# Performance work log

Hardware: AMD Instinct MI355X
Metric: run time of the kernel (lower is better)

The kernel has to match this reference:

```python
import jax, jax.numpy as jnp
import numpy as np

L1, L2, B, D1, D2, HEADS, M = 1024, 1024, 8, 512, 1024, 16, 1024
DPH = M // HEADS  # 64


def setup_inputs() -> dict:
    key = jax.random.key(0)
    ks = jax.random.split(key, 10)
    w = lambda k, shp: jax.random.normal(k, shp, jnp.float32) * 0.02
    z = lambda n: jnp.zeros((n,), jnp.float32)
    return {
        "ctx_1": jax.random.normal(ks[0], (L1, B, D1), jnp.float32),
        "ctx_2": jax.random.normal(ks[1], (L2, B, D2), jnp.float32),
        "Wk1": w(ks[2], (M, D1)), "bk1": z(M),
        "Wv1": w(ks[3], (M, D1)), "bv1": z(M),
        "Wk2": w(ks[4], (M, D2)), "bk2": z(M),
        "Wv2": w(ks[5], (M, D2)), "bv2": z(M),
        "Wf12": w(ks[6], (M, M)), "bf12": z(M),
        "Wf21": w(ks[7], (M, M)), "bf21": z(M),
    }


def _shape_heads(x):
    # [L, B, M] -> [B, H, L, dph]
    L, Bs, _ = x.shape
    return x.reshape(L, Bs, HEADS, DPH).transpose(1, 2, 0, 3)


def _unshape(x):
    # [B, H, L, dph] -> [L, B, M]
    Bs, Hn, L, d = x.shape
    return x.transpose(2, 0, 1, 3).reshape(L, Bs, Hn * d)


def reference(ctx_1, ctx_2, Wk1, bk1, Wv1, bv1, Wk2, bk2, Wv2, bv2,
              Wf12, bf12, Wf21, bf21):
    k1 = _shape_heads(ctx_1 @ Wk1.T + bk1)  # [B,H,L1,d]
    v1 = _shape_heads(ctx_1 @ Wv1.T + bv1)  # [B,H,L1,d]
    k2 = _shape_heads(ctx_2 @ Wk2.T + bk2)  # [B,H,L2,d]
    v2 = _shape_heads(ctx_2 @ Wv2.T + bv2)  # [B,H,L2,d]

    # scores: key_2 @ key_1^T -> [B, H, L2, L1]
    scores = jnp.einsum('bhqd,bhkd->bhqk', k2, k1)

    # direction 1 -> 2: softmax over dim=2 (the L2 axis), then AV with value_1
    dist_1_to_2 = jax.nn.softmax(scores, axis=2)
    context_1_to_2 = jnp.einsum('bhqk,bhkd->bhqd', dist_1_to_2, v1)  # [B,H,L2,d]
    context_1_to_2 = _unshape(context_1_to_2) @ Wf12.T + bf12        # [L2,B,M]

    # direction 2 -> 1: softmax over dim=1 (the head axis), transpose, AV with value_2
    dist_2_to_1 = jax.nn.softmax(scores, axis=1)
    context_2_to_1 = jnp.einsum('bhqk,bhqd->bhkd', dist_2_to_1, v2)  # [B,H,L1,d]
    context_2_to_1 = _unshape(context_2_to_1) @ Wf21.T + bf21        # [L1,B,M]

    return (context_2_to_1, context_1_to_2)
```

## Files before the change

### kernel.cpp

```cpp
#include <hip/hip_runtime.h>
#include <hip/hip_bf16.h>

constexpr int LQ  = 1024;
constexpr int BN  = 8;
constexpr int D1N = 512;
constexpr int D2N = 1024;
constexpr int HN  = 16;
constexpr int MN  = 1024;
constexpr int DPH = 64;

typedef __attribute__((ext_vector_type(8)))  short bf16x8;
typedef __attribute__((ext_vector_type(2)))  float f32x2;
typedef __attribute__((ext_vector_type(4)))  float f32x4;
typedef __attribute__((ext_vector_type(16))) float f32x16;

__device__ __forceinline__ unsigned short f2bf(float f) {
  unsigned u = __float_as_uint(f);
  u += 0x7FFFu + ((u >> 16) & 1u);
  return (unsigned short)(u >> 16);
}
__device__ __forceinline__ float bf2f(unsigned short u) {
  return __uint_as_float(((unsigned)u) << 16);
}
__device__ __forceinline__ float rcpf(float x) {
  float r;
  asm("v_rcp_f32 %0, %1" : "=v"(r) : "v"(x));
  return r;
}

typedef __attribute__((ext_vector_type(4))) float f32x4_;
__device__ __forceinline__ f32x4 mfma16(bf16x8 a, bf16x8 b, f32x4 c) {
  return __builtin_amdgcn_mfma_f32_16x16x32_bf16(a, b, c, 0, 0, 0);
}
__device__ __forceinline__ f32x16 mfma32(bf16x8 a, bf16x8 b, f32x16 c) {
  return __builtin_amdgcn_mfma_f32_32x32x16_bf16(a, b, c, 0, 0, 0);
}
__device__ __forceinline__ f32x16 zero16() {
  f32x16 z;
#pragma unroll
  for (int i = 0; i < 16; ++i) z[i] = 0.f;
  return z;
}

__device__ __forceinline__ unsigned cvtpk(float lo, float hi) {
  unsigned r;
  asm("v_cvt_pk_bf16_f32 %0, %1, %2" : "=v"(r) : "v"(lo), "v"(hi));
  return r;
}

__device__ __forceinline__ void lds_barrier() {
  asm volatile("s_waitcnt lgkmcnt(0)" ::: "memory");
  __builtin_amdgcn_s_barrier();
}

__device__ __forceinline__ bf16x8 pfrag(const float* p) {
  unsigned x0 = cvtpk(p[0], p[1]), y0 = cvtpk(p[4], p[5]);
  unsigned x1 = cvtpk(p[2], p[3]), y1 = cvtpk(p[6], p[7]);
  asm volatile("v_permlane32_swap_b32 %0, %1" : "+v"(x0), "+v"(y0));
  asm volatile("v_permlane32_swap_b32 %0, %1" : "+v"(x1), "+v"(y1));
  union { unsigned u[4]; bf16x8 v; } r;
  r.u[0] = x0; r.u[1] = x1; r.u[2] = y0; r.u[3] = y1;
  return r.v;
}

__device__ __forceinline__ bf16x8 pack8(f32x4 p0, f32x4 p1) {
  bf16x8 o;
  o[0] = (short)f2bf(p0[0]); o[1] = (short)f2bf(p0[1]);
  o[2] = (short)f2bf(p0[2]); o[3] = (short)f2bf(p0[3]);
  o[4] = (short)f2bf(p1[0]); o[5] = (short)f2bf(p1[1]);
  o[6] = (short)f2bf(p1[2]); o[7] = (short)f2bf(p1[3]);
  return o;
}

__global__ __launch_bounds__(256) void cvt_kernel(const float* __restrict__ src,
                                                  unsigned short* __restrict__ dst,
                                                  int n8) {
  int i = blockIdx.x * blockDim.x + threadIdx.x;
  if (i >= n8) return;
  const f32x4* s = (const f32x4*)src;
  f32x4 x = s[2 * i], y = s[2 * i + 1];
  ((bf16x8*)dst)[i] = pack8(x, y);
}

template <int K, int MODE>
__global__ __launch_bounds__(256) void gemm_kernel(const unsigned short* __restrict__ A,
                                                   const unsigned short* __restrict__ W,
                                                   const float* __restrict__ bias,
                                                   void* __restrict__ outp) {
  __shared__ unsigned short As[128 * 40], Bs[128 * 40];
  const int tid = threadIdx.x, wave = tid >> 6, lane = tid & 63;
  const int lg = lane >> 4, lm = lane & 15;
  const int rowb = blockIdx.x * 128, colb = blockIdx.y * 128;
  const int wrow = (wave >> 1) * 64, wcol = (wave & 1) * 64;
  const int sr = tid >> 1, sh = (tid & 1) * 16;
  const unsigned short* Arow = A + (size_t)(rowb + sr) * K + sh;
  const unsigned short* Wrow = W + (size_t)(colb + sr) * K + sh;

  f32x4 acc[4][4];
#pragma unroll
  for (int i = 0; i < 4; ++i)
#pragma unroll
    for (int j = 0; j < 4; ++j) acc[i][j] = (f32x4){0.f, 0.f, 0.f, 0.f};

  bf16x8 a0 = *(const bf16x8*)(Arow);
  bf16x8 a1 = *(const bf16x8*)(Arow + 8);
  bf16x8 b0 = *(const bf16x8*)(Wrow);
  bf16x8 b1 = *(const bf16x8*)(Wrow + 8);

  for (int kk = 0; kk < K; kk += 32) {
    lds_barrier();
    *(bf16x8*)&As[sr * 40 + sh] = a0;
    *(bf16x8*)&As[sr * 40 + sh + 8] = a1;
    *(bf16x8*)&Bs[sr * 40 + sh] = b0;
    *(bf16x8*)&Bs[sr * 40 + sh + 8] = b1;
    const int kn = (kk + 32 < K) ? kk + 32 : 0;
    a0 = *(const bf16x8*)(Arow + kn);
    a1 = *(const bf16x8*)(Arow + kn + 8);
    b0 = *(const bf16x8*)(Wrow + kn);
    b1 = *(const bf16x8*)(Wrow + kn + 8);
    lds_barrier();
    bf16x8 af[4], wf[4];
#pragma unroll
    for (int i = 0; i < 4; ++i) af[i] = *(const bf16x8*)&As[(wrow + i * 16 + lm) * 40 + lg * 8];
#pragma unroll
    for (int j = 0; j < 4; ++j) wf[j] = *(const bf16x8*)&Bs[(wcol + j * 16 + lm) * 40 + lg * 8];
#pragma unroll
    for (int i = 0; i < 4; ++i)
#pragma unroll
      for (int j = 0; j < 4; ++j) acc[i][j] = mfma16(af[i], wf[j], acc[i][j]);
  }

#pragma unroll
  for (int j = 0; j < 4; ++j) {
    int col = colb + wcol + j * 16 + lm;
    float bs = bias[col];
#pragma unroll
    for (int i = 0; i < 4; ++i) {
#pragma unroll
      for (int r = 0; r < 4; ++r) {
        int row = rowb + wrow + i * 16 + lg * 4 + r;
        float v = acc[i][j][r] + bs;
        if (MODE == 0) {
          int l = row >> 3, bb = row & 7, h = col >> 6, d = col & 63;
          ((unsigned short*)outp)[(((size_t)(bb * HN + h)) * LQ + l) * DPH + d] = f2bf(v);
        } else {
          ((float*)outp)[(size_t)row * MN + col] = v;
        }
      }
    }
  }
}

__global__ __launch_bounds__(256) void transpose_kernel(const unsigned short* __restrict__ V,
                                                        unsigned short* __restrict__ VT,
                                                        const float* __restrict__ scale) {
  __shared__ unsigned short t[64][72];
  int bh = blockIdx.y, l0 = blockIdx.x * 64;
  int tid = threadIdx.x;
  int r = tid >> 2, c0 = (tid & 3) * 16;
  const unsigned short* src = V + ((size_t)bh * LQ + l0 + r) * DPH + c0;
  bf16x8 v0 = *(const bf16x8*)(src);
  bf16x8 v1 = *(const bf16x8*)(src + 8);
  if (scale) {
    float sc = scale[(size_t)bh * LQ + l0 + r];
#pragma unroll
    for (int j = 0; j < 8; ++j) {
      v0[j] = (short)f2bf(bf2f((unsigned short)v0[j]) * sc);
      v1[j] = (short)f2bf(bf2f((unsigned short)v1[j]) * sc);
    }
  }
  *(bf16x8*)&t[r][c0] = v0;
  *(bf16x8*)&t[r][c0 + 8] = v1;
  __syncthreads();
  int d = tid >> 2, lc = (tid & 3) * 16;
  bf16x8 o0, o1;
#pragma unroll
  for (int j = 0; j < 8; ++j) {
    o0[j] = (short)t[lc + j][d];
    o1[j] = (short)t[lc + 8 + j][d];
  }
  unsigned short* dst = VT + ((size_t)bh * DPH + d) * LQ + l0 + lc;
  *(bf16x8*)dst = o0;
  *(bf16x8*)(dst + 8) = o1;
}

__global__ __launch_bounds__(256) void col_reduce_kernel(const unsigned short* __restrict__ K1p,
                                                         const unsigned short* __restrict__ K2p,
                                                         float* __restrict__ inv_colsum) {
  int bh = blockIdx.y, kb = blockIdx.x * 128;
  int wave = threadIdx.x >> 6, lane = threadIdx.x & 63, l31 = lane & 31, sg = lane >> 5;
  int k0w = kb + wave * 32;
  const unsigned short* k1 = K1p + (size_t)bh * LQ * DPH;
  const unsigned short* k2 = K2p + (size_t)bh * LQ * DPH;
  bf16x8 bk[4];
#pragma unroll
  for (int i = 0; i < 4; ++i)
    bk[i] = *(const bf16x8*)(k1 + (size_t)(k0w + l31) * DPH + i * 16 + sg * 8);
  float tot = 0.f;
  for (int q0 = 0; q0 < LQ; q0 += 32) {
    bf16x8 aq[4];
#pragma unroll
    for (int i = 0; i < 4; ++i)
      aq[i] = *(const bf16x8*)(k2 + (size_t)(q0 + l31) * DPH + i * 16 + sg * 8);
    f32x16 cs = zero16();
#pragma unroll
    for (int i = 0; i < 4; ++i) cs = mfma32(aq[i], bk[i], cs);
#pragma unroll
    for (int r = 0; r < 16; ++r) tot += __expf(cs[r]);
  }
  tot += __shfl_xor(tot, 32);
  if (lane < 32) inv_colsum[(size_t)bh * LQ + k0w + lane] = 1.0f / tot;
}

__global__ __launch_bounds__(256) void ctx12_kernel(const unsigned short* __restrict__ K1p,
                                                    const unsigned short* __restrict__ K2p,
                                                    const unsigned short* __restrict__ V1Ts,
                                                    unsigned short* __restrict__ c12) {
  int bh = blockIdx.y, b = bh >> 4, h = bh & 15;
  int wave = threadIdx.x >> 6, lane = threadIdx.x & 63, l31 = lane & 31, sg = lane >> 5;
  int q0 = blockIdx.x * 128 + wave * 32;
  const unsigned short* k1 = K1p + (size_t)bh * LQ * DPH;
  const unsigned short* k2 = K2p + (size_t)bh * LQ * DPH;
  const unsigned short* vt = V1Ts + (size_t)bh * DPH * LQ;

  bf16x8 bq[4];
#pragma unroll
  for (int i = 0; i < 4; ++i)
    bq[i] = *(const bf16x8*)(k2 + (size_t)(q0 + l31) * DPH + i * 16 + sg * 8);

  f32x16 acc0 = zero16(), acc1 = zero16();
  for (int k0 = 0; k0 < LQ; k0 += 32) {
    bf16x8 ak[4];
#pragma unroll
    for (int i = 0; i < 4; ++i)
      ak[i] = *(const bf16x8*)(k1 + (size_t)(k0 + l31) * DPH + i * 16 + sg * 8);
    f32x16 cs = zero16();
#pragma unroll
    for (int i = 0; i < 4; ++i) cs = mfma32(ak[i], bq[i], cs);
    float p[16];
#pragma unroll
    for (int r = 0; r < 16; ++r) p[r] = __expf(cs[r]);
    bf16x8 pa0 = pfrag(p), pa1 = pfrag(p + 8);
    bf16x8 v00 = *(const bf16x8*)(vt + (size_t)l31 * LQ + k0 + sg * 8);
    bf16x8 v01 = *(const bf16x8*)(vt + (size_t)l31 * LQ + k0 + 16 + sg * 8);
    bf16x8 v10 = *(const bf16x8*)(vt + (size_t)(32 + l31) * LQ + k0 + sg * 8);
    bf16x8 v11 = *(const bf16x8*)(vt + (size_t)(32 + l31) * LQ + k0 + 16 + sg * 8);
    acc0 = mfma32(pa0, v00, acc0);
    acc0 = mfma32(pa1, v01, acc0);
    acc1 = mfma32(pa0, v10, acc1);
    acc1 = mfma32(pa1, v11, acc1);
  }
#pragma unroll
  for (int r = 0; r < 16; ++r) {
    int q = q0 + (r & 3) + 8 * (r >> 2) + 4 * sg;
    size_t base = ((size_t)q * BN + b) * MN + h * 64;
    c12[base + l31] = f2bf(acc0[r]);
    c12[base + 32 + l31] = f2bf(acc1[r]);
  }
}

__global__ __launch_bounds__(1024) void ctx21_fused_kernel(const unsigned short* __restrict__ K1p,
                                                           const unsigned short* __restrict__ K2p,
                                                           const unsigned short* __restrict__ V2T,
                                                           unsigned short* __restrict__ c21) {
  constexpr int SP = 34;
  constexpr int WS = 32 * SP;
  __shared__ float strip[16 * WS];
  __shared__ float tot[WS];
  const int b = blockIdx.x, kb = blockIdx.y;
  const int tid = threadIdx.x, wave = tid >> 6, lane = tid & 63;
  const int l31 = lane & 31, sg = lane >> 5;
  const int h = wave, bh = b * HN + h;
  const int k0 = kb * 32;
  const unsigned short* k1 = K1p + (size_t)bh * LQ * DPH;
  const unsigned short* k2 = K2p + (size_t)bh * LQ * DPH;
  const unsigned short* vt = V2T + (size_t)bh * DPH * LQ;
  float* mystrip = &strip[wave * WS];

  const int bk_ = tid & 31, bq2 = (tid >> 5) * 2;

  bf16x8 bk[4];
#pragma unroll
  for (int i = 0; i < 4; ++i)
    bk[i] = *(const bf16x8*)(k1 + (size_t)(k0 + l31) * DPH + i * 16 + sg * 8);

  bf16x8 aq[4];
#pragma unroll
  for (int i = 0; i < 4; ++i)
    aq[i] = *(const bf16x8*)(k2 + (size_t)(l31) * DPH + i * 16 + sg * 8);

  f32x16 acc0 = zero16(), acc1 = zero16();

  for (int t = 0; t < LQ / 32; ++t) {
    const int q0 = t * 32;
    f32x16 cs = zero16();
#pragma unroll
    for (int i = 0; i < 4; ++i) cs = mfma32(aq[i], bk[i], cs);
    const int qn = ((t + 1) & 31) * 32;
#pragma unroll
    for (int i = 0; i < 4; ++i)
      aq[i] = *(const bf16x8*)(k2 + (size_t)(qn + l31) * DPH + i * 16 + sg * 8);
    float pex[16];
#pragma unroll
    for (int r = 0; r < 16; ++r) pex[r] = __expf(cs[r]);
#pragma unroll
    for (int g = 0; g < 4; ++g) {
      int qb = g * 8 + 4 * sg;
      *(f32x2*)&mystrip[l31 * SP + qb]     = (f32x2){pex[4 * g],     pex[4 * g + 1]};
      *(f32x2*)&mystrip[l31 * SP + qb + 2] = (f32x2){pex[4 * g + 2], pex[4 * g + 3]};
    }
    bf16x8 v00 = *(const bf16x8*)(vt + (size_t)l31 * LQ + q0 + sg * 8);
    bf16x8 v01 = *(const bf16x8*)(vt + (size_t)l31 * LQ + q0 + 16 + sg * 8);
    bf16x8 v10 = *(const bf16x8*)(vt + (size_t)(32 + l31) * LQ + q0 + sg * 8);
    bf16x8 v11 = *(const bf16x8*)(vt + (size_t)(32 + l31) * LQ + q0 + 16 + sg * 8);
    lds_barrier();
    if (tid < 512) {
      int off = bk_ * SP + bq2;
      f32x2 s = *(const f32x2*)&strip[off];
#pragma unroll
      for (int w = 1; w < 16; ++w) {
        f32x2 v = *(const f32x2*)&strip[w * WS + off];
        s.x += v.x; s.y += v.y;
      }
      f32x2 rc; rc.x = rcpf(s.x); rc.y = rcpf(s.y);
      *(f32x2*)&tot[off] = rc;
    }
    lds_barrier();
    float p8a[8], p8b[8];
#pragma unroll
    for (int g = 0; g < 4; ++g) {
      int qb = g * 8 + 4 * sg;
      f32x2 t0 = *(const f32x2*)&tot[l31 * SP + qb];
      f32x2 t1 = *(const f32x2*)&tot[l31 * SP + qb + 2];
      float* dstp = (g < 2) ? &p8a[(g & 1) * 4] : &p8b[(g & 1) * 4];
      dstp[0] = pex[4 * g]     * t0.x;
      dstp[1] = pex[4 * g + 1] * t0.y;
      dstp[2] = pex[4 * g + 2] * t1.x;
      dstp[3] = pex[4 * g + 3] * t1.y;
    }
    bf16x8 pa0 = pfrag(p8a), pa1 = pfrag(p8b);
    acc0 = mfma32(pa0, v00, acc0);
    acc0 = mfma32(pa1, v01, acc0);
    acc1 = mfma32(pa0, v10, acc1);
    acc1 = mfma32(pa1, v11, acc1);
  }
#pragma unroll
  for (int r = 0; r < 16; ++r) {
    int k = k0 + (r & 3) + 8 * (r >> 2) + 4 * sg;
    size_t base = ((size_t)k * BN + b) * MN + h * 64;
    c21[base + l31] = f2bf(acc0[r]);
    c21[base + 32 + l31] = f2bf(acc1[r]);
  }
}

extern "C" void kernel_launch(void* const* d_in, const int* in_sizes, int n_in,
                              void* d_out, int out_size, void* d_ws, size_t ws_size,
                              hipStream_t stream) {
  const float* ctx1 = (const float*)d_in[0];
  const float* ctx2 = (const float*)d_in[1];
  const float* Wk1 = (const float*)d_in[2];  const float* bk1 = (const float*)d_in[3];
  const float* Wv1 = (const float*)d_in[4];  const float* bv1 = (const float*)d_in[5];
  const float* Wk2 = (const float*)d_in[6];  const float* bk2 = (const float*)d_in[7];
  const float* Wv2 = (const float*)d_in[8];  const float* bv2 = (const float*)d_in[9];
  const float* Wf12 = (const float*)d_in[10]; const float* bf12 = (const float*)d_in[11];
  const float* Wf21 = (const float*)d_in[12]; const float* bf21 = (const float*)d_in[13];

  char* ws = (char*)d_ws;
  size_t off = 0;
  auto alloc = [&](size_t bytes) {
    void* p = ws + off;
    off += (bytes + 255) & ~(size_t)255;
    return p;
  };
  const size_t KV_BYTES = (size_t)BN * HN * LQ * DPH * 2;

  unsigned short* ctx1b = (unsigned short*)alloc((size_t)LQ * BN * D1N * 2);
  unsigned short* ctx2b = (unsigned short*)alloc((size_t)LQ * BN * D2N * 2);
  unsigned short* wk1b = (unsigned short*)alloc((size_t)MN * D1N * 2);
  unsigned short* wv1b = (unsigned short*)alloc((size_t)MN * D1N * 2);
  unsigned short* wk2b = (unsigned short*)alloc((size_t)MN * D2N * 2);
  unsigned short* wv2b = (unsigned short*)alloc((size_t)MN * D2N * 2);
  unsigned short* wf12b = (unsigned short*)alloc((size_t)MN * MN * 2);
  unsigned short* wf21b = (unsigned short*)alloc((size_t)MN * MN * 2);
  unsigned short* K1buf = (unsigned short*)alloc(KV_BYTES);
  unsigned short* K2buf = (unsigned short*)alloc(KV_BYTES);
  unsigned short* V1T = (unsigned short*)alloc(KV_BYTES);
  unsigned short* V2T = (unsigned short*)alloc(KV_BYTES);
  float* invcs = (float*)alloc((size_t)BN * HN * LQ * 4);
  unsigned short* c12 = (unsigned short*)alloc(KV_BYTES);
  unsigned short* c21 = (unsigned short*)alloc(KV_BYTES);
  unsigned short* V1tmp = c12;
  unsigned short* V2tmp = c21;

  auto cvt = [&](const float* s, unsigned short* d, int n) {
    int n8 = n / 8;
    cvt_kernel<<<(n8 + 255) / 256, 256, 0, stream>>>(s, d, n8);
  };
  cvt(ctx1, ctx1b, LQ * BN * D1N);
  cvt(ctx2, ctx2b, LQ * BN * D2N);
  cvt(Wk1, wk1b, MN * D1N);
  cvt(Wv1, wv1b, MN * D1N);
  cvt(Wk2, wk2b, MN * D2N);
  cvt(Wv2, wv2b, MN * D2N);
  cvt(Wf12, wf12b, MN * MN);
  cvt(Wf21, wf21b, MN * MN);

  dim3 gp(64, 8);
  gemm_kernel<D1N, 0><<<gp, 256, 0, stream>>>(ctx1b, wk1b, bk1, K1buf);
  gemm_kernel<D1N, 0><<<gp, 256, 0, stream>>>(ctx1b, wv1b, bv1, V1tmp);
  gemm_kernel<D2N, 0><<<gp, 256, 0, stream>>>(ctx2b, wk2b, bk2, K2buf);
  gemm_kernel<D2N, 0><<<gp, 256, 0, stream>>>(ctx2b, wv2b, bv2, V2tmp);

  col_reduce_kernel<<<dim3(LQ / 128, BN * HN), 256, 0, stream>>>(K1buf, K2buf, invcs);
  dim3 gt(LQ / 64, BN * HN);
  transpose_kernel<<<gt, 256, 0, stream>>>(V1tmp, V1T, invcs);
  transpose_kernel<<<gt, 256, 0, stream>>>(V2tmp, V2T, nullptr);

  ctx12_kernel<<<dim3(LQ / 128, BN * HN), 256, 0, stream>>>(K1buf, K2buf, V1T, c12);
  ctx21_fused_kernel<<<dim3(BN, LQ / 32), 1024, 0, stream>>>(K1buf, K2buf, V2T, c21);

  float* out0 = (float*)d_out;
  float* out1 = out0 + (size_t)LQ * BN * MN;
  gemm_kernel<MN, 2><<<gp, 256, 0, stream>>>(c21, wf21b, bf21, out0);
  gemm_kernel<MN, 2><<<gp, 256, 0, stream>>>(c12, wf12b, bf12, out1);
}
```

Before: 481.9 us.

## Fuse input bf16 conversion into projection GEMMs, merge GEMM launches, widen ctx21 tile

```diff
diff --git a/kernel.cpp b/kernel.cpp
--- a/kernel.cpp
+++ b/kernel.cpp
@@ -28,7 +28,6 @@
   return r;
 }
 
-typedef __attribute__((ext_vector_type(4))) float f32x4_;
 __device__ __forceinline__ f32x4 mfma16(bf16x8 a, bf16x8 b, f32x4 c) {
   return __builtin_amdgcn_mfma_f32_16x16x32_bf16(a, b, c, 0, 0, 0);
 }
@@ -71,6 +70,12 @@
   o[6] = (short)f2bf(p1[2]); o[7] = (short)f2bf(p1[3]);
   return o;
 }
+__device__ __forceinline__ bf16x8 pack8q(f32x4 lo, f32x4 hi) {
+  union { unsigned u[4]; bf16x8 v; } r;
+  r.u[0] = cvtpk(lo[0], lo[1]); r.u[1] = cvtpk(lo[2], lo[3]);
+  r.u[2] = cvtpk(hi[0], hi[1]); r.u[3] = cvtpk(hi[2], hi[3]);
+  return r.v;
+}
 
 __global__ __launch_bounds__(256) void cvt_kernel(const float* __restrict__ src,
                                                   unsigned short* __restrict__ dst,
@@ -82,18 +87,21 @@
   ((bf16x8*)dst)[i] = pack8(x, y);
 }
 
-template <int K, int MODE>
-__global__ __launch_bounds__(256) void gemm_kernel(const unsigned short* __restrict__ A,
-                                                   const unsigned short* __restrict__ W,
-                                                   const float* __restrict__ bias,
-                                                   void* __restrict__ outp) {
+template <int K, int MODE, bool AF32>
+__device__ __forceinline__ void gemm_body(const void* __restrict__ Ap,
+                                          const unsigned short* __restrict__ W,
+                                          const float* __restrict__ bias,
+                                          void* __restrict__ outp,
+                                          int rowb, int colb) {
   __shared__ unsigned short As[128 * 40], Bs[128 * 40];
   const int tid = threadIdx.x, wave = tid >> 6, lane = tid & 63;
   const int lg = lane >> 4, lm = lane & 15;
-  const int rowb = blockIdx.x * 128, colb = blockIdx.y * 128;
   const int wrow = (wave >> 1) * 64, wcol = (wave & 1) * 64;
   const int sr = tid >> 1, sh = (tid & 1) * 16;
-  const unsigned short* Arow = A + (size_t)(rowb + sr) * K + sh;
+  const unsigned short* Arow = AF32 ? nullptr
+      : (const unsigned short*)Ap + (size_t)(rowb + sr) * K + sh;
+  const float* ArowF = AF32 ? (const float*)Ap + (size_t)(rowb + sr) * K + sh
+                            : nullptr;
   const unsigned short* Wrow = W + (size_t)(colb + sr) * K + sh;
 
   f32x4 acc[4][4];
@@ -102,20 +110,37 @@
 #pragma unroll
     for (int j = 0; j < 4; ++j) acc[i][j] = (f32x4){0.f, 0.f, 0.f, 0.f};
 
-  bf16x8 a0 = *(const bf16x8*)(Arow);
-  bf16x8 a1 = *(const bf16x8*)(Arow + 8);
-  bf16x8 b0 = *(const bf16x8*)(Wrow);
-  bf16x8 b1 = *(const bf16x8*)(Wrow + 8);
+  f32x4 fa0, fa1, fa2, fa3;
+  bf16x8 a0, a1, b0, b1;
+  if (AF32) {
+    fa0 = *(const f32x4*)(ArowF);     fa1 = *(const f32x4*)(ArowF + 4);
+    fa2 = *(const f32x4*)(ArowF + 8); fa3 = *(const f32x4*)(ArowF + 12);
+  } else {
+    a0 = *(const bf16x8*)(Arow);
+    a1 = *(const bf16x8*)(Arow + 8);
+  }
+  b0 = *(const bf16x8*)(Wrow);
+  b1 = *(const bf16x8*)(Wrow + 8);
 
   for (int kk = 0; kk < K; kk += 32) {
     lds_barrier();
-    *(bf16x8*)&As[sr * 40 + sh] = a0;
-    *(bf16x8*)&As[sr * 40 + sh + 8] = a1;
+    if (AF32) {
+      *(bf16x8*)&As[sr * 40 + sh]     = pack8q(fa0, fa1);
+      *(bf16x8*)&As[sr * 40 + sh + 8] = pack8q(fa2, fa3);
+    } else {
+      *(bf16x8*)&As[sr * 40 + sh] = a0;
+      *(bf16x8*)&As[sr * 40 + sh + 8] = a1;
+    }
     *(bf16x8*)&Bs[sr * 40 + sh] = b0;
     *(bf16x8*)&Bs[sr * 40 + sh + 8] = b1;
     const int kn = (kk + 32 < K) ? kk + 32 : 0;
-    a0 = *(const bf16x8*)(Arow + kn);
-    a1 = *(const bf16x8*)(Arow + kn + 8);
+    if (AF32) {
+      fa0 = *(const f32x4*)(ArowF + kn);     fa1 = *(const f32x4*)(ArowF + kn + 4);
+      fa2 = *(const f32x4*)(ArowF + kn + 8); fa3 = *(const f32x4*)(ArowF + kn + 12);
+    } else {
+      a0 = *(const bf16x8*)(Arow + kn);
+      a1 = *(const bf16x8*)(Arow + kn + 8);
+    }
     b0 = *(const bf16x8*)(Wrow + kn);
     b1 = *(const bf16x8*)(Wrow + kn + 8);
     lds_barrier();
@@ -149,6 +174,28 @@
       }
     }
   }
+}
+
+template <int K>
+__global__ __launch_bounds__(256) void gemm_pair_f32_kernel(
+    const float* __restrict__ A,
+    const unsigned short* __restrict__ W0, const unsigned short* __restrict__ W1,
+    const float* __restrict__ b0, const float* __restrict__ b1,
+    void* __restrict__ o0, void* __restrict__ o1) {
+  const int sel = blockIdx.x & 1;
+  gemm_body<K, 0, true>(A, sel ? W1 : W0, sel ? b1 : b0, sel ? o1 : o0,
+                        (blockIdx.x >> 1) * 128, blockIdx.y * 128);
+}
+
+template <int K>
+__global__ __launch_bounds__(256) void gemm_dual_kernel(
+    const unsigned short* __restrict__ A0, const unsigned short* __restrict__ A1,
+    const unsigned short* __restrict__ W0, const unsigned short* __restrict__ W1,
+    const float* __restrict__ b0, const float* __restrict__ b1,
+    void* __restrict__ o0, void* __restrict__ o1) {
+  const int sel = blockIdx.y >> 3;
+  gemm_body<K, 2, false>(sel ? A1 : A0, sel ? W1 : W0, sel ? b1 : b0,
+                         sel ? o1 : o0, blockIdx.x * 128, (blockIdx.y & 7) * 128);
 }
 
 __global__ __launch_bounds__(256) void transpose_kernel(const unsigned short* __restrict__ V,
@@ -263,7 +310,7 @@
                                                            const unsigned short* __restrict__ K2p,
                                                            const unsigned short* __restrict__ V2T,
                                                            unsigned short* __restrict__ c21) {
-  constexpr int SP = 34;
+  constexpr int SP = 66;
   constexpr int WS = 32 * SP;
   __shared__ float strip[16 * WS];
   __shared__ float tot[WS];
@@ -277,72 +324,101 @@
   const unsigned short* vt = V2T + (size_t)bh * DPH * LQ;
   float* mystrip = &strip[wave * WS];
 
-  const int bk_ = tid & 31, bq2 = (tid >> 5) * 2;
+  const int boff = (tid >> 5) * SP + 2 * (tid & 31);
 
   bf16x8 bk[4];
 #pragma unroll
   for (int i = 0; i < 4; ++i)
     bk[i] = *(const bf16x8*)(k1 + (size_t)(k0 + l31) * DPH + i * 16 + sg * 8);
 
-  bf16x8 aq[4];
-#pragma unroll
-  for (int i = 0; i < 4; ++i)
-    aq[i] = *(const bf16x8*)(k2 + (size_t)(l31) * DPH + i * 16 + sg * 8);
-
   f32x16 acc0 = zero16(), acc1 = zero16();
 
-  for (int t = 0; t < LQ / 32; ++t) {
-    const int q0 = t * 32;
-    f32x16 cs = zero16();
-#pragma unroll
-    for (int i = 0; i < 4; ++i) cs = mfma32(aq[i], bk[i], cs);
-    const int qn = ((t + 1) & 31) * 32;
-#pragma unroll
-    for (int i = 0; i < 4; ++i)
-      aq[i] = *(const bf16x8*)(k2 + (size_t)(qn + l31) * DPH + i * 16 + sg * 8);
-    float pex[16];
-#pragma unroll
-    for (int r = 0; r < 16; ++r) pex[r] = __expf(cs[r]);
-#pragma unroll
-    for (int g = 0; g < 4; ++g) {
-      int qb = g * 8 + 4 * sg;
-      *(f32x2*)&mystrip[l31 * SP + qb]     = (f32x2){pex[4 * g],     pex[4 * g + 1]};
-      *(f32x2*)&mystrip[l31 * SP + qb + 2] = (f32x2){pex[4 * g + 2], pex[4 * g + 3]};
-    }
+  for (int t = 0; t < LQ / 64; ++t) {
+    const int q0 = t * 64;
     bf16x8 v00 = *(const bf16x8*)(vt + (size_t)l31 * LQ + q0 + sg * 8);
     bf16x8 v01 = *(const bf16x8*)(vt + (size_t)l31 * LQ + q0 + 16 + sg * 8);
     bf16x8 v10 = *(const bf16x8*)(vt + (size_t)(32 + l31) * LQ + q0 + sg * 8);
     bf16x8 v11 = *(const bf16x8*)(vt + (size_t)(32 + l31) * LQ + q0 + 16 + sg * 8);
+    {
+      bf16x8 aqlo[4], aqhi[4];
+#pragma unroll
+      for (int i = 0; i < 4; ++i) {
+        aqlo[i] = *(const bf16x8*)(k2 + (size_t)(q0 + l31) * DPH + i * 16 + sg * 8);
+        aqhi[i] = *(const bf16x8*)(k2 + (size_t)(q0 + 32 + l31) * DPH + i * 16 + sg * 8);
+      }
+      f32x16 cs = zero16();
+#pragma unroll
+      for (int i = 0; i < 4; ++i) cs = mfma32(aqlo[i], bk[i], cs);
+#pragma unroll
+      for (int g = 0; g < 4; ++g) {
+        int qb = g * 8 + 4 * sg;
+        *(f32x2*)&mystrip[l31 * SP + qb]     = (f32x2){__expf(cs[4 * g]),     __expf(cs[4 * g + 1])};
+        *(f32x2*)&mystrip[l31 * SP + qb + 2] = (f32x2){__expf(cs[4 * g + 2]), __expf(cs[4 * g + 3])};
+      }
+      f32x16 cs2 = zero16();
+#pragma unroll
+      for (int i = 0; i < 4; ++i) cs2 = mfma32(aqhi[i], bk[i], cs2);
+#pragma unroll
+      for (int g = 0; g < 4; ++g) {
+        int qb = 32 + g * 8 + 4 * sg;
+        *(f32x2*)&mystrip[l31 * SP + qb]     = (f32x2){__expf(cs2[4 * g]),     __expf(cs2[4 * g + 1])};
+        *(f32x2*)&mystrip[l31 * SP + qb + 2] = (f32x2){__expf(cs2[4 * g + 2]), __expf(cs2[4 * g + 3])};
+      }
+    }
     lds_barrier();
-    if (tid < 512) {
-      int off = bk_ * SP + bq2;
-      f32x2 s = *(const f32x2*)&strip[off];
+    bf16x8 v20 = *(const bf16x8*)(vt + (size_t)l31 * LQ + q0 + 32 + sg * 8);
+    bf16x8 v21 = *(const bf16x8*)(vt + (size_t)l31 * LQ + q0 + 48 + sg * 8);
+    bf16x8 v30 = *(const bf16x8*)(vt + (size_t)(32 + l31) * LQ + q0 + 32 + sg * 8);
+    bf16x8 v31 = *(const bf16x8*)(vt + (size_t)(32 + l31) * LQ + q0 + 48 + sg * 8);
+    {
+      f32x2 s = *(const f32x2*)&strip[boff];
 #pragma unroll
       for (int w = 1; w < 16; ++w) {
-        f32x2 v = *(const f32x2*)&strip[w * WS + off];
+        f32x2 v = *(const f32x2*)&strip[w * WS + boff];
         s.x += v.x; s.y += v.y;
       }
       f32x2 rc; rc.x = rcpf(s.x); rc.y = rcpf(s.y);
-      *(f32x2*)&tot[off] = rc;
+      *(f32x2*)&tot[boff] = rc;
     }
     lds_barrier();
-    float p8a[8], p8b[8];
-#pragma unroll
-    for (int g = 0; g < 4; ++g) {
-      int qb = g * 8 + 4 * sg;
-      f32x2 t0 = *(const f32x2*)&tot[l31 * SP + qb];
-      f32x2 t1 = *(const f32x2*)&tot[l31 * SP + qb + 2];
-      float* dstp = (g < 2) ? &p8a[(g & 1) * 4] : &p8b[(g & 1) * 4];
-      dstp[0] = pex[4 * g]     * t0.x;
-      dstp[1] = pex[4 * g + 1] * t0.y;
-      dstp[2] = pex[4 * g + 2] * t1.x;
-      dstp[3] = pex[4 * g + 3] * t1.y;
-    }
-    bf16x8 pa0 = pfrag(p8a), pa1 = pfrag(p8b);
-    acc0 = mfma32(pa0, v00, acc0);
-    acc0 = mfma32(pa1, v01, acc0);
-    acc1 = mfma32(pa0, v10, acc1);
-    acc1 = mfma32(pa1, v11, acc1);
+    {
+      float p8a[8], p8b[8];
+#pragma unroll
+      for (int g = 0; g < 4; ++g) {
+        int qb = g * 8 + 4 * sg;
+        f32x2 e0 = *(const f32x2*)&mystrip[l31 * SP + qb];
+        f32x2 e1 = *(const f32x2*)&mystrip[l31 * SP + qb + 2];
+        f32x2 i0 = *(const f32x2*)&tot[l31 * SP + qb];
+        f32x2 i1 = *(const f32x2*)&tot[l31 * SP + qb + 2];
+        float* dstp = (g < 2) ? &p8a[(g & 1) * 4] : &p8b[(g & 1) * 4];
+        dstp[0] = e0.x * i0.x; dstp[1] = e0.y * i0.y;
+        dstp[2] = e1.x * i1.x; dstp[3] = e1.y * i1.y;
+      }
+      bf16x8 pa0 = pfrag(p8a), pa1 = pfrag(p8b);
+      acc0 = mfma32(pa0, v00, acc0);
+      acc0 = mfma32(pa1, v01, acc0);
+      acc1 = mfma32(pa0, v10, acc1);
+      acc1 = mfma32(pa1, v11, acc1);
+    }
+    {
+      float p8c[8], p8d[8];
+#pragma unroll
+      for (int g = 0; g < 4; ++g) {
+        int qb = 32 + g * 8 + 4 * sg;
+        f32x2 e0 = *(const f32x2*)&mystrip[l31 * SP + qb];
+        f32x2 e1 = *(const f32x2*)&mystrip[l31 * SP + qb + 2];
+        f32x2 i0 = *(const f32x2*)&tot[l31 * SP + qb];
+        f32x2 i1 = *(const f32x2*)&tot[l31 * SP + qb + 2];
+        float* dstp = (g < 2) ? &p8c[(g & 1) * 4] : &p8d[(g & 1) * 4];
+        dstp[0] = e0.x * i0.x; dstp[1] = e0.y * i0.y;
+        dstp[2] = e1.x * i1.x; dstp[3] = e1.y * i1.y;
+      }
+      bf16x8 pa2 = pfrag(p8c), pa3 = pfrag(p8d);
+      acc0 = mfma32(pa2, v20, acc0);
+      acc0 = mfma32(pa3, v21, acc0);
+      acc1 = mfma32(pa2, v30, acc1);
+      acc1 = mfma32(pa3, v31, acc1);
+    }
   }
 #pragma unroll
   for (int r = 0; r < 16; ++r) {
@@ -374,8 +450,6 @@
   };
   const size_t KV_BYTES = (size_t)BN * HN * LQ * DPH * 2;
 
-  unsigned short* ctx1b = (unsigned short*)alloc((size_t)LQ * BN * D1N * 2);
-  unsigned short* ctx2b = (unsigned short*)alloc((size_t)LQ * BN * D2N * 2);
   unsigned short* wk1b = (unsigned short*)alloc((size_t)MN * D1N * 2);
   unsigned short* wv1b = (unsigned short*)alloc((size_t)MN * D1N * 2);
   unsigned short* wk2b = (unsigned short*)alloc((size_t)MN * D2N * 2);
@@ -396,8 +470,6 @@
     int n8 = n / 8;
     cvt_kernel<<<(n8 + 255) / 256, 256, 0, stream>>>(s, d, n8);
   };
-  cvt(ctx1, ctx1b, LQ * BN * D1N);
-  cvt(ctx2, ctx2b, LQ * BN * D2N);
   cvt(Wk1, wk1b, MN * D1N);
   cvt(Wv1, wv1b, MN * D1N);
   cvt(Wk2, wk2b, MN * D2N);
@@ -405,11 +477,10 @@
   cvt(Wf12, wf12b, MN * MN);
   cvt(Wf21, wf21b, MN * MN);
 
-  dim3 gp(64, 8);
-  gemm_kernel<D1N, 0><<<gp, 256, 0, stream>>>(ctx1b, wk1b, bk1, K1buf);
-  gemm_kernel<D1N, 0><<<gp, 256, 0, stream>>>(ctx1b, wv1b, bv1, V1tmp);
-  gemm_kernel<D2N, 0><<<gp, 256, 0, stream>>>(ctx2b, wk2b, bk2, K2buf);
-  gemm_kernel<D2N, 0><<<gp, 256, 0, stream>>>(ctx2b, wv2b, bv2, V2tmp);
+  gemm_pair_f32_kernel<D1N><<<dim3(128, 8), 256, 0, stream>>>(
+      ctx1, wk1b, wv1b, bk1, bv1, K1buf, V1tmp);
+  gemm_pair_f32_kernel<D2N><<<dim3(128, 8), 256, 0, stream>>>(
+      ctx2, wk2b, wv2b, bk2, bv2, K2buf, V2tmp);
 
   col_reduce_kernel<<<dim3(LQ / 128, BN * HN), 256, 0, stream>>>(K1buf, K2buf, invcs);
   dim3 gt(LQ / 64, BN * HN);
@@ -421,6 +492,6 @@
 
   float* out0 = (float*)d_out;
   float* out1 = out0 + (size_t)LQ * BN * MN;
-  gemm_kernel<MN, 2><<<gp, 256, 0, stream>>>(c21, wf21b, bf21, out0);
-  gemm_kernel<MN, 2><<<gp, 256, 0, stream>>>(c12, wf12b, bf12, out1);
-}
+  gemm_dual_kernel<MN><<<dim3(64, 16), 256, 0, stream>>>(
+      c21, c12, wf21b, wf12b, bf21, bf12, out0, out1);
+}
```

Result: no change. 486.4 us (+0.9%).
